# Performance work log

Hardware: AMD Instinct MI355X
Metric: run time of the kernel (lower is better)

Reference implementation:

```python
import jax, jax.numpy as jnp
import numpy as np

B, C, H, W = 2, 128, 64, 64
CR4 = C // 4  # hidden width of linear_weight / bias branches
SOFTMAX_SCALE = 1.0


def _leaky(z):
    return jnp.where(z >= 0, z, 0.2 * z)


def _conv1x1(x, w, b):
    # x: [B,Ci,H,W], w: [Co,Ci], b: [Co]
    return jnp.einsum('oc,bchw->bohw', w, x) + b[None, :, None, None]


def setup_inputs() -> dict:
    key = jax.random.key(0)
    ks = jax.random.split(key, 16)
    def n(k, shape, s=0.05):
        return jax.random.normal(k, shape, jnp.float32) * s
    return {
        'x': jax.random.normal(ks[0], (B, C, H, W), jnp.float32),
        'value_w': n(ks[1], (C, C)), 'value_b': n(ks[2], (C,)),
        'query_w': n(ks[3], (C, C)), 'query_b': n(ks[4], (C,)),
        'lw1_w': n(ks[5], (CR4, C)), 'lw1_b': n(ks[6], (CR4,)),
        'lw2_w': n(ks[7], (1, CR4)), 'lw2_b': n(ks[8], (1,)),
        'bi1_w': n(ks[9], (CR4, C)), 'bi1_b': n(ks[10], (CR4,)),
        'bi2_w': n(ks[11], (1, CR4)), 'bi2_b': n(ks[12], (1,)),
        'lin_w': n(ks[13], (C, C, 3, 3)), 'lin_b': n(ks[14], (C,)),
    }


def reference(x, value_w, value_b, query_w, query_b,
              lw1_w, lw1_b, lw2_w, lw2_b,
              bi1_w, bi1_b, bi2_w, bi2_b,
              lin_w, lin_b):
    # value / query 1x1 projections
    x1 = _conv1x1(x, value_w, value_b)   # [B,C,H,W]
    x2 = _conv1x1(x, query_w, query_b)   # [B,C,H,W]
    # dynamic per-pixel weight / bias maps (two 1x1 convs + LeakyReLU)
    wei = _conv1x1(_leaky(_conv1x1(x2, lw1_w, lw1_b)), lw2_w, lw2_b)  # [B,1,H,W]
    bii = _conv1x1(_leaky(_conv1x1(x2, bi1_w, bi1_b)), bi2_w, bi2_b)  # [B,1,H,W]

    Bn, Cn, Hn, Wn = x.shape
    L = Hn * Wn  # one 1x1 patch per spatial location (ksize=1, stride=1)
    # query patches [B,L,C]; normalize each patch to (at least 1e-4) unit norm
    wq = x2.transpose(0, 2, 3, 1).reshape(Bn, L, Cn)
    wnorm = wq / jnp.maximum(jnp.linalg.norm(wq, axis=2, keepdims=True), 1e-4)
    # attention scores: per-sample conv2d(xi, wi_normed) == batched matmul
    yi = jnp.einsum('bchw,blc->blhw', x2, wnorm)  # [B,L,H,W]
    # sparse gating
    sparse = jax.nn.relu(yi - yi.mean(axis=1, keepdims=True) * wei + bii)
    sr = (sparse != 0.0).astype(yi.dtype)
    yi = yi * sparse
    yi = jax.nn.softmax(yi * SOFTMAX_SCALE, axis=1)
    yi = jnp.maximum(yi * sr, 1e-8)
    # reconstruct with value patches (conv_transpose2d with 1x1 kernels)
    raw = x1.transpose(0, 2, 3, 1).reshape(Bn, L, Cn)
    out = jnp.einsum('blhw,blc->bchw', yi, raw)  # / (ksize*ksize) == /1
    # final 3x3 conv + LeakyReLU + residual
    y = jax.lax.conv_general_dilated(out, lin_w, (1, 1), 'SAME',
                                     dimension_numbers=('NCHW', 'OIHW', 'NCHW'))
    y = _leaky(y + lin_b[None, :, None, None])
    return y + x
```

## Files before the change

kernel.cpp:

```cpp
#include <hip/hip_runtime.h>
#include <hip/hip_bf16.h>
#include <math.h>

#define BB 2
#define C 128
#define L 4096
#define CR4 32
#define RS 4

typedef unsigned short ushort_t;
typedef __attribute__((ext_vector_type(8))) short s16x8;
typedef __attribute__((ext_vector_type(4))) float f32x4;

__device__ inline float leaky(float z) { return (z >= 0.f) ? z : 0.2f * z; }

__device__ inline unsigned short f2bf(float f) {
    unsigned int u = __builtin_bit_cast(unsigned int, f);
    unsigned int r = (u + 0x7fffu + ((u >> 16) & 1u)) >> 16;
    return (unsigned short)r;
}
__device__ inline float bf2f(unsigned short b) {
    unsigned int u = ((unsigned int)b) << 16;
    return __builtin_bit_cast(float, u);
}
__device__ inline unsigned int cvtpk(float lo, float hi) {
    unsigned int r;
    asm("v_cvt_pk_bf16_f32 %0, %1, %2" : "=v"(r) : "v"(lo), "v"(hi));
    return r;
}

__global__ __launch_bounds__(256) void k_wcomp(
    const float* __restrict__ vw, const float* __restrict__ vb,
    const float* __restrict__ qw, const float* __restrict__ qb,
    const float* __restrict__ lw1w, const float* __restrict__ lw1b,
    const float* __restrict__ bi1w, const float* __restrict__ bi1b,
    ushort_t* __restrict__ WQV, float* __restrict__ biasv)
{
    const int mt = blockIdx.x;
    const int t = threadIdx.x;
    const int kk = t >> 6, lane = t & 63;
    const int row = mt * 16 + (lane & 15);
    const int k0 = kk * 32 + (lane >> 4) * 8;
    s16x8 v;
    if (row < 128) {
        #pragma unroll
        for (int j = 0; j < 8; ++j) v[j] = (short)f2bf(vw[row * 128 + k0 + j]);
    } else if (row < 256) {
        #pragma unroll
        for (int j = 0; j < 8; ++j) v[j] = (short)f2bf(qw[(row - 128) * 128 + k0 + j]);
    } else {
        const float* w1 = (row < 288) ? lw1w + (row - 256) * 128
                                      : bi1w + (row - 288) * 128;
        float acc[8] = {0.f, 0.f, 0.f, 0.f, 0.f, 0.f, 0.f, 0.f};
        #pragma unroll 2
        for (int k = 0; k < 128; ++k) {
            float wv_ = w1[k];
            const float* qr = qw + k * 128 + k0;
            #pragma unroll
            for (int j = 0; j < 8; ++j) acc[j] = fmaf(wv_, qr[j], acc[j]);
        }
        #pragma unroll
        for (int j = 0; j < 8; ++j) v[j] = (short)f2bf(acc[j]);
    }
    *(s16x8*)(WQV + ((size_t)(mt * 4 + kk) * 64 + lane) * 8) = v;

    if (t < 16) {
        int rr = mt * 16 + t;
        float bv;
        if (rr < 128) bv = vb[rr];
        else if (rr < 256) bv = qb[rr - 128];
        else {
            const float* w1 = (rr < 288) ? lw1w + (rr - 256) * 128
                                         : bi1w + (rr - 288) * 128;
            float a = (rr < 288) ? lw1b[rr - 256] : bi1b[rr - 288];
            for (int k = 0; k < 128; ++k) a = fmaf(w1[k], qb[k], a);
            bv = a;
        }
        biasv[rr] = bv;
    }
}

__global__ __launch_bounds__(256, 1) void k_proj2(
    const float* __restrict__ x, const ushort_t* __restrict__ WQV,
    const float* __restrict__ biasv,
    const float* __restrict__ lw2w, const float* __restrict__ lw2b,
    const float* __restrict__ bi2w, const float* __restrict__ bi2b,
    ushort_t* __restrict__ x2a, ushort_t* __restrict__ x1g,
    float* __restrict__ weiA, float* __restrict__ biiA, float* __restrict__ scA,
    float* __restrict__ cpart)
{
    __shared__ __align__(16) char smem[16384 + 1536];
    char* xT = smem;
    float* biasLDS = (float*)(smem + 16384);
    float* w2LDS = biasLDS + 320;

    const int t = threadIdx.x;
    const int blk = blockIdx.x;
    const int part = blockIdx.y;
    const int b = blk >> 6;
    const int p0 = (blk & 63) * 64;
    const int wv = t >> 6, lane = t & 63, n = lane & 15, g = lane >> 4;

    biasLDS[t] = biasv[t];
    if (t < 64) {
        biasLDS[256 + t] = biasv[256 + t];
        w2LDS[t] = (t < 32) ? lw2w[t] : bi2w[t - 32];
    }

    const int pl = t & 63, cg = t >> 6;
    const float* xb = x + (size_t)b * C * L + p0 + pl;
    #pragma unroll
    for (int i = 0; i < 16; ++i) {
        int c = cg * 32 + i * 2;
        float v0 = xb[(size_t)c * L];
        float v1 = xb[(size_t)(c + 1) * L];
        int slot = c >> 3;
        int offs = (c * 2) & 15;
        int byte = pl * 256 + (((slot ^ (pl & 15)) << 4) | offs);
        *(unsigned int*)(xT + byte) = cvtpk(v0, v1);
    }
    __syncthreads();

    const int brow = wv * 16 + n;
    const int p = p0 + wv * 16 + n;
    const size_t bL = (size_t)b * L;

    if (part == 0) {
        const int mtm[12] = {0, 1, 2, 3, 4, 5, 6, 7, 16, 17, 18, 19};
        f32x4 acc[12];
        #pragma unroll
        for (int i = 0; i < 12; ++i) acc[i] = (f32x4){0.f, 0.f, 0.f, 0.f};
        #pragma unroll
        for (int kk = 0; kk < 4; ++kk) {
            const s16x8 bfr = *(const s16x8*)(xT + brow * 256 + (((4 * kk + g) ^ n) << 4));
            #pragma unroll
            for (int i = 0; i < 12; ++i) {
                const s16x8 afr = *(const s16x8*)(WQV + ((size_t)(mtm[i] * 4 + kk) * 64 + lane) * 8);
                acc[i] = __builtin_amdgcn_mfma_f32_16x16x32_bf16(afr, bfr, acc[i], 0, 0, 0);
            }
        }
        #pragma unroll
        for (int i = 0; i < 12; ++i) {
            const f32x4 bv = *(const f32x4*)(biasLDS + mtm[i] * 16 + g * 4);
            acc[i][0] += bv[0]; acc[i][1] += bv[1];
            acc[i][2] += bv[2]; acc[i][3] += bv[3];
        }
        #pragma unroll
        for (int i = 0; i < 8; ++i)
            #pragma unroll
            for (int r = 0; r < 4; ++r)
                x1g[((size_t)b * C + i * 16 + g * 4 + r) * L + p] = f2bf(acc[i][r]);
        float pw = 0.f, pbb = 0.f;
        #pragma unroll
        for (int i = 8; i < 10; ++i)
            #pragma unroll
            for (int r = 0; r < 4; ++r)
                pw = fmaf(w2LDS[(i - 8) * 16 + g * 4 + r], leaky(acc[i][r]), pw);
        #pragma unroll
        for (int i = 10; i < 12; ++i)
            #pragma unroll
            for (int r = 0; r < 4; ++r)
                pbb = fmaf(w2LDS[32 + (i - 10) * 16 + g * 4 + r], leaky(acc[i][r]), pbb);
        pw += __shfl_xor(pw, 16, 64);  pw += __shfl_xor(pw, 32, 64);
        pbb += __shfl_xor(pbb, 16, 64); pbb += __shfl_xor(pbb, 32, 64);
        if (g == 0) {
            weiA[bL + p] = pw + lw2b[0];
            biiA[bL + p] = pbb + bi2b[0];
        }
    } else {
        f32x4 acc[8];
        #pragma unroll
        for (int i = 0; i < 8; ++i) acc[i] = (f32x4){0.f, 0.f, 0.f, 0.f};
        #pragma unroll
        for (int kk = 0; kk < 4; ++kk) {
            const s16x8 bfr = *(const s16x8*)(xT + brow * 256 + (((4 * kk + g) ^ n) << 4));
            #pragma unroll
            for (int i = 0; i < 8; ++i) {
                const s16x8 afr = *(const s16x8*)(WQV + ((size_t)((8 + i) * 4 + kk) * 64 + lane) * 8);
                acc[i] = __builtin_amdgcn_mfma_f32_16x16x32_bf16(afr, bfr, acc[i], 0, 0, 0);
            }
        }
        #pragma unroll
        for (int i = 0; i < 8; ++i) {
            const f32x4 bv = *(const f32x4*)(biasLDS + (8 + i) * 16 + g * 4);
            acc[i][0] += bv[0]; acc[i][1] += bv[1];
            acc[i][2] += bv[2]; acc[i][3] += bv[3];
        }
        float pn = 0.f;
        #pragma unroll
        for (int i = 0; i < 8; ++i)
            #pragma unroll
            for (int r = 0; r < 4; ++r) pn = fmaf(acc[i][r], acc[i][r], pn);
        pn += __shfl_xor(pn, 16, 64);
        pn += __shfl_xor(pn, 32, 64);
        float scv = fmaxf(sqrtf(pn), 1e-4f);
        float dinv = 1.f / scv;
        if (g == 0) scA[bL + p] = scv;
        #pragma unroll
        for (int i = 0; i < 8; ++i) {
            uint2 uu;
            uu.x = cvtpk(acc[i][0] * dinv, acc[i][1] * dinv);
            uu.y = cvtpk(acc[i][2] * dinv, acc[i][3] * dinv);
            *(uint2*)(x2a + (bL + p) * C + i * 16 + g * 4) = uu;
        }
        float sv[32];
        #pragma unroll
        for (int i = 0; i < 8; ++i)
            #pragma unroll
            for (int r = 0; r < 4; ++r)
                sv[i * 4 + r] = acc[i][r] * dinv;
        #pragma unroll
        for (int mask = 1; mask <= 8; mask <<= 1)
            #pragma unroll
            for (int i = 0; i < 32; ++i)
                sv[i] += __shfl_xor(sv[i], mask, 64);
        __syncthreads();
        float* sumsh = (float*)xT;
        if (n == 0) {
            #pragma unroll
            for (int i = 0; i < 32; ++i) {
                int ch = (i >> 2) * 16 + g * 4 + (i & 3);
                sumsh[wv * 128 + ch] = sv[i];
            }
        }
        __syncthreads();
        if (t < 128)
            cpart[(size_t)blk * 128 + t] =
                (sumsh[t] + sumsh[128 + t]) + (sumsh[256 + t] + sumsh[384 + t]);
    }
}

__global__ __launch_bounds__(256, 2) void k_attn(
    const ushort_t* __restrict__ x2a, const ushort_t* __restrict__ x1g,
    const float* __restrict__ scA, const float* __restrict__ weiA,
    const float* __restrict__ biiA, const float* __restrict__ cpart,
    ushort_t* __restrict__ Opb, float* __restrict__ Mp, float* __restrict__ Zp)
{
    __shared__ __align__(16) char smem[73728];
    __shared__ float cbsh[128];

    const int t = threadIdx.x;
    const int w = t >> 6, lane = t & 63, n = lane & 15, g = lane >> 4;
    char* Pw = smem + 65536 + w * 2048;

    const int blk = blockIdx.x;
    const int q = blk & (RS - 1);
    const int colt = (blk >> 2) & 63;
    const int b = blk >> 8;
    const int p = colt * 64 + w * 16 + n;
    const size_t bL = (size_t)b * L;

    if (t < 128) {
        float s = 0.f;
        const float* cp = cpart + (size_t)(b * 64) * 128 + t;
        #pragma unroll 4
        for (int j = 0; j < 64; ++j) s += cp[(size_t)j * 128];
        cbsh[t] = s * (1.f / (float)L);
    }

    const int l0base = q * (L / RS);
    const char* x2src = (const char*)(x2a + (bL + l0base) * C);
    const char* x1src = (const char*)(x1g + (size_t)b * C * L);

    #define STAGE_X2(buf, tile_)                                                         \
        {   const char* sb = x2src + (size_t)(tile_) * 64 * 256;                          \
            _Pragma("unroll")                                                             \
            for (int rr = 0; rr < 4; ++rr) {                                              \
                int slot = rr * 256 + t;                                                  \
                int lrow = slot >> 4, uu = slot & 15;                                     \
                const char* gp = sb + lrow * 256 + (((uu ^ (lrow & 7))) << 4);            \
                char* lp = (buf) + ((rr * 256 + w * 64) << 4);                            \
                __builtin_amdgcn_global_load_lds(                                         \
                    (const __attribute__((address_space(1))) unsigned int*)gp,            \
                    (__attribute__((address_space(3))) unsigned int*)lp, 16, 0, 0);       \
            } }
    #define STAGE_X1(buf, l0_)                                                            \
        {   _Pragma("unroll")                                                             \
            for (int rr = 0; rr < 4; ++rr) {                                              \
                int slot = rr * 256 + t;                                                  \
                int cr = slot >> 3, uu = slot & 7;                                        \
                const char* gp = x1src + ((size_t)cr * L + (l0_) + ((uu ^ (cr & 7)) << 3)) * 2; \
                char* lp = (buf) + ((rr * 256 + w * 64) << 4);                            \
                __builtin_amdgcn_global_load_lds(                                         \
                    (const __attribute__((address_space(1))) unsigned int*)gp,            \
                    (__attribute__((address_space(3))) unsigned int*)lp, 16, 0, 0);       \
            } }

    char* Abuf0 = smem;          char* Abuf1 = smem + 16384;
    char* Xbuf0 = smem + 32768;  char* Xbuf1 = smem + 49152;

    STAGE_X2(Abuf0, 0);
    STAGE_X1(Xbuf0, l0base);
    __syncthreads();

    const s16x8* qrow = (const s16x8*)(x2a + (bL + p) * C);
    const float scp = scA[bL + p];
    s16x8 bq[4];
    float dot = 0.f;
    #pragma unroll
    for (int kk = 0; kk < 4; ++kk) {
        s16x8 raw = qrow[kk * 4 + g];
        const float* cbp = cbsh + kk * 32 + g * 8;
        s16x8 u;
        #pragma unroll
        for (int j = 0; j < 8; ++j) {
            float rv = bf2f((unsigned short)raw[j]) * scp;
            u[j] = (short)f2bf(rv);
            dot = fmaf(cbp[j], rv, dot);
        }
        bq[kk] = u;
    }
    dot += __shfl_xor(dot, 16, 64);
    dot += __shfl_xor(dot, 32, 64);
    const float tq = fmaf(weiA[bL + p], dot, -biiA[bL + p]);

    f32x4 Oacc[8];
    #pragma unroll
    for (int ct = 0; ct < 8; ++ct) Oacc[ct] = (f32x4){0.f, 0.f, 0.f, 0.f};
    float Mrun = 0.f, Zrun = 0.f;

    const int swz = n & 7;
    const int NT = L / RS / 64;

    #pragma unroll 1
    for (int tile = 0; tile < NT; ++tile) {
        char* Ab = (tile & 1) ? Abuf1 : Abuf0;
        char* Xb = (tile & 1) ? Xbuf1 : Xbuf0;
        if (tile + 1 < NT) {
            char* An = (tile & 1) ? Abuf0 : Abuf1;
            char* Xn = (tile & 1) ? Xbuf0 : Xbuf1;
            STAGE_X2(An, tile + 1);
            STAGE_X1(Xn, l0base + (tile + 1) * 64);
        }

        f32x4 s4[4];
        #pragma unroll
        for (int lt = 0; lt < 4; ++lt) s4[lt] = (f32x4){0.f, 0.f, 0.f, 0.f};
        __builtin_amdgcn_s_setprio(1);
        #pragma unroll
        for (int kk = 0; kk < 4; ++kk) {
            #pragma unroll
            for (int lt = 0; lt < 4; ++lt) {
                const s16x8 a = *(const s16x8*)(Ab + (16 * lt + n) * 256 +
                                                (((4 * kk + g) ^ swz) << 4));
                s4[lt] = __builtin_amdgcn_mfma_f32_16x16x32_bf16(a, bq[kk], s4[lt], 0, 0, 0);
            }
        }
        __builtin_amdgcn_s_setprio(0);

        float vv[16], sps[16];
        #pragma unroll
        for (int lt = 0; lt < 4; ++lt) {
            #pragma unroll
            for (int r = 0; r < 4; ++r) {
                float s = s4[lt][r];
                float sp = s - tq;
                sps[lt * 4 + r] = sp;
                vv[lt * 4 + r] = s * fmaxf(sp, 0.f);
            }
        }
        float tm[8];
        #pragma unroll
        for (int i = 0; i < 8; ++i) tm[i] = fmaxf(vv[2 * i], vv[2 * i + 1]);
        #pragma unroll
        for (int i = 0; i < 4; ++i) tm[i] = fmaxf(tm[2 * i], tm[2 * i + 1]);
        float tmax = fmaxf(fmaxf(tm[0], tm[1]), fmaxf(tm[2], tm[3]));
        tmax = fmaxf(tmax, __shfl_xor(tmax, 16, 64));
        tmax = fmaxf(tmax, __shfl_xor(tmax, 32, 64));

        if (!__all(tmax <= Mrun + 8.f)) {
            float Mn = fmaxf(Mrun, tmax);
            float so = __expf(Mrun - Mn);
            Mrun = Mn;
            Zrun *= so;
            #pragma unroll
            for (int ct = 0; ct < 8; ++ct) {
                Oacc[ct][0] *= so; Oacc[ct][1] *= so;
                Oacc[ct][2] *= so; Oacc[ct][3] *= so;
            }
        }

        #pragma unroll
        for (int lt = 0; lt < 4; ++lt) {
            float e0 = __expf(vv[lt * 4 + 0] - Mrun);
            float e1 = __expf(vv[lt * 4 + 1] - Mrun);
            float e2 = __expf(vv[lt * 4 + 2] - Mrun);
            float e3 = __expf(vv[lt * 4 + 3] - Mrun);
            Zrun += (e0 + e1) + (e2 + e3);
            float p0 = sps[lt * 4 + 0] > 0.f ? e0 : 0.f;
            float p1 = sps[lt * 4 + 1] > 0.f ? e1 : 0.f;
            float p2 = sps[lt * 4 + 2] > 0.f ? e2 : 0.f;
            float p3 = sps[lt * 4 + 3] > 0.f ? e3 : 0.f;
            int ulog = 2 * lt + (g >> 1);
            int byte = n * 128 + ((ulog ^ swz) << 4) + ((g & 1) << 3);
            uint2 uu;
            uu.x = cvtpk(p0, p1);
            uu.y = cvtpk(p2, p3);
            *(uint2*)(Pw + byte) = uu;
        }

        __builtin_amdgcn_s_setprio(1);
        #pragma unroll
        for (int kk2 = 0; kk2 < 2; ++kk2) {
            const s16x8 pb = *(const s16x8*)(Pw + n * 128 + (((4 * kk2 + g) ^ swz) << 4));
            #pragma unroll
            for (int ct = 0; ct < 8; ++ct) {
                const s16x8 a = *(const s16x8*)(Xb + (16 * ct + n) * 128 +
                                                (((4 * kk2 + g) ^ swz) << 4));
                Oacc[ct] = __builtin_amdgcn_mfma_f32_16x16x32_bf16(a, pb, Oacc[ct], 0, 0, 0);
            }
        }
        __builtin_amdgcn_s_setprio(0);
        __syncthreads();
    }
    #undef STAGE_X2
    #undef STAGE_X1

    float z = Zrun;
    z += __shfl_xor(z, 16, 64);
    z += __shfl_xor(z, 32, 64);

    const size_t sset = (size_t)(q * BB + b);
    ushort_t* ob = Opb + (sset * L + p) * C;
    #pragma unroll
    for (int ct = 0; ct < 8; ++ct) {
        uint2 uu;
        uu.x = cvtpk(Oacc[ct][0], Oacc[ct][1]);
        uu.y = cvtpk(Oacc[ct][2], Oacc[ct][3]);
        *(uint2*)(ob + 16 * ct + 4 * g) = uu;
    }
    if (g == 0) {
        Mp[sset * L + p] = Mrun;
        Zp[sset * L + p] = z;
    }
}

__global__ __launch_bounds__(256) void k_mergewrep(
    const ushort_t* __restrict__ Opb, const float* __restrict__ Mp,
    const float* __restrict__ Zp, ushort_t* __restrict__ attnb,
    const float* __restrict__ lw, ushort_t* __restrict__ W3)
{
    const int blkid = blockIdx.x;
    const int t = threadIdx.x;
    if (blkid < 1024) {
        const int idx = blkid * 256 + t;
        const int c4 = idx & 31;
        const int p = (idx >> 5) & 4095;
        const int b = idx >> 17;
        size_t is[RS];
        float M = -1e30f;
        float Mq[RS], Zq[RS];
        #pragma unroll
        for (int q = 0; q < RS; ++q) {
            is[q] = (size_t)(q * BB + b) * L + p;
            Mq[q] = Mp[is[q]];
            Zq[q] = Zp[is[q]];
            M = fmaxf(M, Mq[q]);
        }
        float Zt = 0.f;
        float aq[RS];
        #pragma unroll
        for (int q = 0; q < RS; ++q) {
            aq[q] = __expf(Mq[q] - M);
            Zt = fmaf(Zq[q], aq[q], Zt);
        }
        float zi = 1.f / Zt;
        float r0 = 0.f, r1 = 0.f, r2 = 0.f, r3 = 0.f;
        #pragma unroll
        for (int q = 0; q < RS; ++q) {
            float s = aq[q] * zi;
            const ushort4 o = *(const ushort4*)(Opb + is[q] * C + c4 * 4);
            r0 = fmaf(bf2f(o.x), s, r0);
            r1 = fmaf(bf2f(o.y), s, r1);
            r2 = fmaf(bf2f(o.z), s, r2);
            r3 = fmaf(bf2f(o.w), s, r3);
        }
        uint2 uu;
        uu.x = cvtpk(r0, r1);
        uu.y = cvtpk(r2, r3);
        *(uint2*)(attnb + ((size_t)b * L + p) * C + c4 * 4) = uu;
    } else {
        const int tid = (blkid - 1024) * 256 + t;
        const int s = tid >> 9;
        const int r = tid & 511;
        const int mt = r >> 6, lane = r & 63;
        const int co = mt * 16 + (lane & 15), g = lane >> 4;
        const int kk = s >> 2, kc = s & 3;
        const int ci0 = kc * 32 + g * 8;
        s16x8 v;
        #pragma unroll
        for (int j = 0; j < 8; ++j)
            v[j] = (short)f2bf(lw[((size_t)co * 128 + ci0 + j) * 9 + kk]);
        *(s16x8*)(W3 + (size_t)tid * 8) = v;
    }
}

__global__ __launch_bounds__(256, 1) void k_conv(
    const ushort_t* __restrict__ attnb, const float* __restrict__ x,
    const ushort_t* __restrict__ W3, const float* __restrict__ lb,
    float* __restrict__ out)
{
    __shared__ __align__(16) char attnT[49152];

    const int t = threadIdx.x;
    const int wv = t >> 6, lane = t & 63, n = lane & 15, g = lane >> 4;
    const int h = blockIdx.x;
    const int half = blockIdx.y;
    const int b = blockIdx.z;

    const char* asrc = (const char*)attnb + ((size_t)b * L + (size_t)(h - 1) * 64) * C * 2;
    #pragma unroll
    for (int rr = 0; rr < 3; ++rr) {
        if ((unsigned)(h - 1 + rr) < 64u) {
            #pragma unroll
            for (int qq = 0; qq < 4; ++qq) {
                int slot = rr * 1024 + qq * 256 + t;
                int lrow = slot >> 4, uu = slot & 15;
                const char* gp = asrc + lrow * 256 + ((uu ^ (lrow & 7)) << 4);
                char* lp = attnT + ((rr * 1024 + qq * 256 + wv * 64) << 4);
                __builtin_amdgcn_global_load_lds(
                    (const __attribute__((address_space(1))) unsigned int*)gp,
                    (__attribute__((address_space(3))) unsigned int*)lp, 16, 0, 0);
            }
        }
    }

    #define WROW(s_, mi_) (*(const s16x8*)(W3 + (((size_t)(s_) * 8 + 2 * wv + (mi_)) * 64 + lane) * 8))

    s16x8 w0a = WROW(0, 0), w0b = WROW(0, 1);
    s16x8 w1a = WROW(1, 0), w1b = WROW(1, 1);

    __syncthreads();

    f32x4 acc[2][2];
    #pragma unroll
    for (int mi = 0; mi < 2; ++mi)
        #pragma unroll
        for (int nt = 0; nt < 2; ++nt) acc[mi][nt] = (f32x4){0.f, 0.f, 0.f, 0.f};

    const s16x8 zer = {0, 0, 0, 0, 0, 0, 0, 0};

    #define CONV_STEP(s_, af0_, af1_)                                                    \
    {   const int kk = (s_) >> 2, kc = (s_) & 3;                                         \
        const int kh = kk / 3, kw = kk - kh * 3;                                         \
        const int dh = kh - 1, dw = kw - 1;                                              \
        const bool hval = ((unsigned)(h + dh) < 64u);                                    \
        _Pragma("unroll")                                                                \
        for (int nt = 0; nt < 2; ++nt) {                                                 \
            int pl = half * 32 + nt * 16 + n;                                            \
            int wd = pl + dw;                                                            \
            bool val = hval && ((unsigned)wd < 64u);                                     \
            int wc = wd < 0 ? 0 : (wd > 63 ? 63 : wd);                                   \
            int lrow = (dh + 1) * 64 + wc;                                               \
            s16x8 bf_ = *(const s16x8*)(attnT + lrow * 256 +                             \
                                        (((kc * 4 + g) ^ (lrow & 7)) << 4));             \
            if (!val) bf_ = zer;                                                         \
            acc[0][nt] = __builtin_amdgcn_mfma_f32_16x16x32_bf16(af0_, bf_, acc[0][nt], 0, 0, 0); \
            acc[1][nt] = __builtin_amdgcn_mfma_f32_16x16x32_bf16(af1_, bf_, acc[1][nt], 0, 0, 0); \
        }                                                                                \
    }

    #pragma unroll 1
    for (int s = 0; s < 36; s += 2) {
        s16x8 af0 = w0a, af1 = w0b;
        if (s + 2 < 36) { w0a = WROW(s + 2, 0); w0b = WROW(s + 2, 1); }
        CONV_STEP(s, af0, af1)
        af0 = w1a; af1 = w1b;
        if (s + 3 < 36) { w1a = WROW(s + 3, 0); w1b = WROW(s + 3, 1); }
        CONV_STEP(s + 1, af0, af1)
    }
    #undef CONV_STEP
    #undef WROW

    const float* xb = x + (size_t)b * C * L + h * 64;
    float* ob = out + (size_t)b * C * L + h * 64;
    #pragma unroll
    for (int mi = 0; mi < 2; ++mi) {
        #pragma unroll
        for (int r = 0; r < 4; ++r) {
            int co = (2 * wv + mi) * 16 + g * 4 + r;
            float bias = lb[co];
            #pragma unroll
            for (int nt = 0; nt < 2; ++nt) {
                int p_ = half * 32 + nt * 16 + n;
                float v = leaky(acc[mi][nt][r] + bias);
                ob[(size_t)co * L + p_] = v + xb[(size_t)co * L + p_];
            }
        }
    }
}

extern "C" void kernel_launch(void* const* d_in, const int* in_sizes, int n_in,
                              void* d_out, int out_size, void* d_ws, size_t ws_size,
                              hipStream_t stream) {
    const float* x     = (const float*)d_in[0];
    const float* vw    = (const float*)d_in[1];
    const float* vb    = (const float*)d_in[2];
    const float* qw    = (const float*)d_in[3];
    const float* qb    = (const float*)d_in[4];
    const float* lw1w  = (const float*)d_in[5];
    const float* lw1b  = (const float*)d_in[6];
    const float* lw2w  = (const float*)d_in[7];
    const float* lw2b  = (const float*)d_in[8];
    const float* bi1w  = (const float*)d_in[9];
    const float* bi1b  = (const float*)d_in[10];
    const float* bi2w  = (const float*)d_in[11];
    const float* bi2b  = (const float*)d_in[12];
    const float* lw    = (const float*)d_in[13];
    const float* lb    = (const float*)d_in[14];
    float* out = (float*)d_out;

    char* ws = (char*)d_ws;
    ushort_t* x2a  = (ushort_t*)ws;
    ushort_t* x1g  = (ushort_t*)(ws + 2097152);
    ushort_t* Opb  = (ushort_t*)(ws + 4194304);
    ushort_t* WQV  = (ushort_t*)(ws + 4194304);
    float* biasv = (float*)(ws + 4194304 + 81920);
    float* weiA  = (float*)(ws + 12582912);
    float* biiA  = weiA + BB * L;
    float* scA   = biiA + BB * L;
    float* Mp    = scA + BB * L;
    float* Zp    = Mp + RS * BB * L;
    float* cpart = Zp + RS * BB * L;
    ushort_t* W3 = x1g;
    ushort_t* attnb = x2a;

    hipLaunchKernelGGL(k_wcomp, dim3(20), dim3(256), 0, stream,
                       vw, vb, qw, qb, lw1w, lw1b, bi1w, bi1b, WQV, biasv);

    hipLaunchKernelGGL(k_proj2, dim3(128, 2), dim3(256), 0, stream,
                       x, WQV, biasv, lw2w, lw2b, bi2w, bi2b,
                       x2a, x1g, weiA, biiA, scA, cpart);

    hipLaunchKernelGGL(k_attn, dim3(BB * 64 * RS), dim3(256), 0, stream,
                       x2a, x1g, scA, weiA, biiA, cpart, Opb, Mp, Zp);

    hipLaunchKernelGGL(k_mergewrep, dim3(1096), dim3(256), 0, stream,
                       Opb, Mp, Zp, attnb, lw, W3);

    hipLaunchKernelGGL(k_conv, dim3(64, 2, BB), dim3(256), 0, stream,
                       attnb, x, W3, lb, out);
}
```

Before: 99.51 us.

## Give each attention wave two query column groups to reuse staged tiles

The attention kernel now runs 128 threads per block, and each wave handles two 16-query column groups (A and B) instead of one. The key and value LDS fragments are loaded into registers once per tile and reused for both query sets, which halves LDS reads per unit of MFMA work. The price is much higher register pressure (two sets of output accumulators plus 32 cached fragments) and launch bounds reduced to one block. Fewer waves per block also means each thread stages twice as many global-to-LDS loads.

```diff
diff --git a/kernel.cpp b/kernel.cpp
--- a/kernel.cpp
+++ b/kernel.cpp
@@ -230,7 +230,7 @@
     }
 }
 
-__global__ __launch_bounds__(256, 2) void k_attn(
+__global__ __launch_bounds__(128, 1) void k_attn(
     const ushort_t* __restrict__ x2a, const ushort_t* __restrict__ x1g,
     const float* __restrict__ scA, const float* __restrict__ weiA,
     const float* __restrict__ biiA, const float* __restrict__ cpart,
@@ -241,22 +241,16 @@
 
     const int t = threadIdx.x;
     const int w = t >> 6, lane = t & 63, n = lane & 15, g = lane >> 4;
-    char* Pw = smem + 65536 + w * 2048;
+    char* PwA = smem + 65536 + (w * 2) * 2048;
+    char* PwB = PwA + 2048;
 
     const int blk = blockIdx.x;
     const int q = blk & (RS - 1);
     const int colt = (blk >> 2) & 63;
     const int b = blk >> 8;
-    const int p = colt * 64 + w * 16 + n;
+    const int pA = colt * 64 + w * 16 + n;
+    const int pB = pA + 32;
     const size_t bL = (size_t)b * L;
-
-    if (t < 128) {
-        float s = 0.f;
-        const float* cp = cpart + (size_t)(b * 64) * 128 + t;
-        #pragma unroll 4
-        for (int j = 0; j < 64; ++j) s += cp[(size_t)j * 128];
-        cbsh[t] = s * (1.f / (float)L);
-    }
 
     const int l0base = q * (L / RS);
     const char* x2src = (const char*)(x2a + (bL + l0base) * C);
@@ -265,22 +259,22 @@
     #define STAGE_X2(buf, tile_)                                                         \
         {   const char* sb = x2src + (size_t)(tile_) * 64 * 256;                          \
             _Pragma("unroll")                                                             \
-            for (int rr = 0; rr < 4; ++rr) {                                              \
-                int slot = rr * 256 + t;                                                  \
+            for (int rr = 0; rr < 8; ++rr) {                                              \
+                int slot = rr * 128 + t;                                                  \
                 int lrow = slot >> 4, uu = slot & 15;                                     \
                 const char* gp = sb + lrow * 256 + (((uu ^ (lrow & 7))) << 4);            \
-                char* lp = (buf) + ((rr * 256 + w * 64) << 4);                            \
+                char* lp = (buf) + ((rr * 128 + w * 64) << 4);                            \
                 __builtin_amdgcn_global_load_lds(                                         \
                     (const __attribute__((address_space(1))) unsigned int*)gp,            \
                     (__attribute__((address_space(3))) unsigned int*)lp, 16, 0, 0);       \
             } }
     #define STAGE_X1(buf, l0_)                                                            \
         {   _Pragma("unroll")                                                             \
-            for (int rr = 0; rr < 4; ++rr) {                                              \
-                int slot = rr * 256 + t;                                                  \
+            for (int rr = 0; rr < 8; ++rr) {                                              \
+                int slot = rr * 128 + t;                                                  \
                 int cr = slot >> 3, uu = slot & 7;                                        \
                 const char* gp = x1src + ((size_t)cr * L + (l0_) + ((uu ^ (cr & 7)) << 3)) * 2; \
-                char* lp = (buf) + ((rr * 256 + w * 64) << 4);                            \
+                char* lp = (buf) + ((rr * 128 + w * 64) << 4);                            \
                 __builtin_amdgcn_global_load_lds(                                         \
                     (const __attribute__((address_space(1))) unsigned int*)gp,            \
                     (__attribute__((address_space(3))) unsigned int*)lp, 16, 0, 0);       \
@@ -291,36 +285,128 @@
 
     STAGE_X2(Abuf0, 0);
     STAGE_X1(Xbuf0, l0base);
+
+    {
+        float s = 0.f;
+        const float* cp = cpart + (size_t)(b * 64) * 128 + t;
+        #pragma unroll 4
+        for (int j = 0; j < 64; ++j) s += cp[(size_t)j * 128];
+        cbsh[t] = s * (1.f / (float)L);
+    }
     __syncthreads();
 
-    const s16x8* qrow = (const s16x8*)(x2a + (bL + p) * C);
-    const float scp = scA[bL + p];
-    s16x8 bq[4];
-    float dot = 0.f;
+    s16x8 bqA[4], bqB[4];
+    float tqA, tqB;
+    {
+        const s16x8* qrow = (const s16x8*)(x2a + (bL + pA) * C);
+        const float scp = scA[bL + pA];
+        float dot = 0.f;
+        #pragma unroll
+        for (int kk = 0; kk < 4; ++kk) {
+            s16x8 raw = qrow[kk * 4 + g];
+            const float* cbp = cbsh + kk * 32 + g * 8;
+            s16x8 u;
+            #pragma unroll
+            for (int j = 0; j < 8; ++j) {
+                float rv = bf2f((unsigned short)raw[j]) * scp;
+                u[j] = (short)f2bf(rv);
+                dot = fmaf(cbp[j], rv, dot);
+            }
+            bqA[kk] = u;
+        }
+        dot += __shfl_xor(dot, 16, 64);
+        dot += __shfl_xor(dot, 32, 64);
+        tqA = fmaf(weiA[bL + pA], dot, -biiA[bL + pA]);
+    }
+    {
+        const s16x8* qrow = (const s16x8*)(x2a + (bL + pB) * C);
+        const float scp = scA[bL + pB];
+        float dot = 0.f;
+        #pragma unroll
+        for (int kk = 0; kk < 4; ++kk) {
+            s16x8 raw = qrow[kk * 4 + g];
+            const float* cbp = cbsh + kk * 32 + g * 8;
+            s16x8 u;
+            #pragma unroll
+            for (int j = 0; j < 8; ++j) {
+                float rv = bf2f((unsigned short)raw[j]) * scp;
+                u[j] = (short)f2bf(rv);
+                dot = fmaf(cbp[j], rv, dot);
+            }
+            bqB[kk] = u;
+        }
+        dot += __shfl_xor(dot, 16, 64);
+        dot += __shfl_xor(dot, 32, 64);
+        tqB = fmaf(weiA[bL + pB], dot, -biiA[bL + pB]);
+    }
+
+    f32x4 OA[8], OB[8];
     #pragma unroll
-    for (int kk = 0; kk < 4; ++kk) {
-        s16x8 raw = qrow[kk * 4 + g];
-        const float* cbp = cbsh + kk * 32 + g * 8;
-        s16x8 u;
-        #pragma unroll
-        for (int j = 0; j < 8; ++j) {
-            float rv = bf2f((unsigned short)raw[j]) * scp;
-            u[j] = (short)f2bf(rv);
-            dot = fmaf(cbp[j], rv, dot);
-        }
-        bq[kk] = u;
-    }
-    dot += __shfl_xor(dot, 16, 64);
-    dot += __shfl_xor(dot, 32, 64);
-    const float tq = fmaf(weiA[bL + p], dot, -biiA[bL + p]);
-
-    f32x4 Oacc[8];
-    #pragma unroll
-    for (int ct = 0; ct < 8; ++ct) Oacc[ct] = (f32x4){0.f, 0.f, 0.f, 0.f};
-    float Mrun = 0.f, Zrun = 0.f;
+    for (int ct = 0; ct < 8; ++ct) {
+        OA[ct] = (f32x4){0.f, 0.f, 0.f, 0.f};
+        OB[ct] = (f32x4){0.f, 0.f, 0.f, 0.f};
+    }
+    float MrunA = 0.f, ZrunA = 0.f, MrunB = 0.f, ZrunB = 0.f;
 
     const int swz = n & 7;
     const int NT = L / RS / 64;
+
+    #define SOFTPV(sX, tqX, MrunX, ZrunX, OX, PwX)                                       \
+    {   float vv[16], sps[16];                                                           \
+        _Pragma("unroll")                                                                \
+        for (int lt = 0; lt < 4; ++lt) {                                                 \
+            _Pragma("unroll")                                                            \
+            for (int r = 0; r < 4; ++r) {                                                \
+                float s_ = sX[lt][r];                                                    \
+                float sp = s_ - tqX;                                                     \
+                sps[lt * 4 + r] = sp;                                                    \
+                vv[lt * 4 + r] = s_ * fmaxf(sp, 0.f);                                    \
+            }                                                                            \
+        }                                                                                \
+        float tm[8];                                                                     \
+        _Pragma("unroll")                                                                \
+        for (int i = 0; i < 8; ++i) tm[i] = fmaxf(vv[2 * i], vv[2 * i + 1]);             \
+        _Pragma("unroll")                                                                \
+        for (int i = 0; i < 4; ++i) tm[i] = fmaxf(tm[2 * i], tm[2 * i + 1]);             \
+        float tmax = fmaxf(fmaxf(tm[0], tm[1]), fmaxf(tm[2], tm[3]));                    \
+        tmax = fmaxf(tmax, __shfl_xor(tmax, 16, 64));                                    \
+        tmax = fmaxf(tmax, __shfl_xor(tmax, 32, 64));                                    \
+        if (!__all(tmax <= MrunX + 8.f)) {                                               \
+            float Mn = fmaxf(MrunX, tmax);                                               \
+            float so = __expf(MrunX - Mn);                                               \
+            MrunX = Mn;                                                                  \
+            ZrunX *= so;                                                                 \
+            _Pragma("unroll")                                                            \
+            for (int ct = 0; ct < 8; ++ct) {                                             \
+                OX[ct][0] *= so; OX[ct][1] *= so;                                        \
+                OX[ct][2] *= so; OX[ct][3] *= so;                                        \
+            }                                                                            \
+        }                                                                                \
+        _Pragma("unroll")                                                                \
+        for (int lt = 0; lt < 4; ++lt) {                                                 \
+            float e0 = __expf(vv[lt * 4 + 0] - MrunX);                                   \
+            float e1 = __expf(vv[lt * 4 + 1] - MrunX);                                   \
+            float e2 = __expf(vv[lt * 4 + 2] - MrunX);                                   \
+            float e3 = __expf(vv[lt * 4 + 3] - MrunX);                                   \
+            ZrunX += (e0 + e1) + (e2 + e3);                                              \
+            float p0_ = sps[lt * 4 + 0] > 0.f ? e0 : 0.f;                                \
+            float p1_ = sps[lt * 4 + 1] > 0.f ? e1 : 0.f;                                \
+            float p2_ = sps[lt * 4 + 2] > 0.f ? e2 : 0.f;                                \
+            float p3_ = sps[lt * 4 + 3] > 0.f ? e3 : 0.f;                                \
+            int ulog = 2 * lt + (g >> 1);                                                \
+            int byte = n * 128 + ((ulog ^ swz) << 4) + ((g & 1) << 3);                   \
+            *(unsigned int*)((PwX) + byte)     = cvtpk(p0_, p1_);                        \
+            *(unsigned int*)((PwX) + byte + 4) = cvtpk(p2_, p3_);                        \
+        }                                                                                \
+        _Pragma("unroll")                                                                \
+        for (int kk2 = 0; kk2 < 2; ++kk2) {                                              \
+            const s16x8 pb = *(const s16x8*)((PwX) + n * 128 + (((4 * kk2 + g) ^ swz) << 4)); \
+            _Pragma("unroll")                                                            \
+            for (int ct = 0; ct < 8; ++ct)                                               \
+                OX[ct] = __builtin_amdgcn_mfma_f32_16x16x32_bf16(xf[kk2 * 8 + ct], pb,   \
+                                                                 OX[ct], 0, 0, 0);       \
+        }                                                                                \
+    }
 
     #pragma unroll 1
     for (int tile = 0; tile < NT; ++tile) {
@@ -333,105 +419,74 @@
             STAGE_X1(Xn, l0base + (tile + 1) * 64);
         }
 
-        f32x4 s4[4];
-        #pragma unroll
-        for (int lt = 0; lt < 4; ++lt) s4[lt] = (f32x4){0.f, 0.f, 0.f, 0.f};
+        s16x8 af[16];
+        #pragma unroll
+        for (int kk = 0; kk < 4; ++kk)
+            #pragma unroll
+            for (int lt = 0; lt < 4; ++lt)
+                af[kk * 4 + lt] = *(const s16x8*)(Ab + (16 * lt + n) * 256 +
+                                                  (((4 * kk + g) ^ swz) << 4));
+        f32x4 sA[4], sB[4];
+        #pragma unroll
+        for (int lt = 0; lt < 4; ++lt) {
+            sA[lt] = (f32x4){0.f, 0.f, 0.f, 0.f};
+            sB[lt] = (f32x4){0.f, 0.f, 0.f, 0.f};
+        }
         __builtin_amdgcn_s_setprio(1);
         #pragma unroll
-        for (int kk = 0; kk < 4; ++kk) {
-            #pragma unroll
-            for (int lt = 0; lt < 4; ++lt) {
-                const s16x8 a = *(const s16x8*)(Ab + (16 * lt + n) * 256 +
-                                                (((4 * kk + g) ^ swz) << 4));
-                s4[lt] = __builtin_amdgcn_mfma_f32_16x16x32_bf16(a, bq[kk], s4[lt], 0, 0, 0);
-            }
-        }
+        for (int kk = 0; kk < 4; ++kk)
+            #pragma unroll
+            for (int lt = 0; lt < 4; ++lt)
+                sA[lt] = __builtin_amdgcn_mfma_f32_16x16x32_bf16(af[kk * 4 + lt], bqA[kk], sA[lt], 0, 0, 0);
+        #pragma unroll
+        for (int kk = 0; kk < 4; ++kk)
+            #pragma unroll
+            for (int lt = 0; lt < 4; ++lt)
+                sB[lt] = __builtin_amdgcn_mfma_f32_16x16x32_bf16(af[kk * 4 + lt], bqB[kk], sB[lt], 0, 0, 0);
         __builtin_amdgcn_s_setprio(0);
 
-        float vv[16], sps[16];
-        #pragma unroll
-        for (int lt = 0; lt < 4; ++lt) {
-            #pragma unroll
-            for (int r = 0; r < 4; ++r) {
-                float s = s4[lt][r];
-                float sp = s - tq;
-                sps[lt * 4 + r] = sp;
-                vv[lt * 4 + r] = s * fmaxf(sp, 0.f);
-            }
-        }
-        float tm[8];
-        #pragma unroll
-        for (int i = 0; i < 8; ++i) tm[i] = fmaxf(vv[2 * i], vv[2 * i + 1]);
-        #pragma unroll
-        for (int i = 0; i < 4; ++i) tm[i] = fmaxf(tm[2 * i], tm[2 * i + 1]);
-        float tmax = fmaxf(fmaxf(tm[0], tm[1]), fmaxf(tm[2], tm[3]));
-        tmax = fmaxf(tmax, __shfl_xor(tmax, 16, 64));
-        tmax = fmaxf(tmax, __shfl_xor(tmax, 32, 64));
-
-        if (!__all(tmax <= Mrun + 8.f)) {
-            float Mn = fmaxf(Mrun, tmax);
-            float so = __expf(Mrun - Mn);
-            Mrun = Mn;
-            Zrun *= so;
-            #pragma unroll
-            for (int ct = 0; ct < 8; ++ct) {
-                Oacc[ct][0] *= so; Oacc[ct][1] *= so;
-                Oacc[ct][2] *= so; Oacc[ct][3] *= so;
-            }
-        }
-
-        #pragma unroll
-        for (int lt = 0; lt < 4; ++lt) {
-            float e0 = __expf(vv[lt * 4 + 0] - Mrun);
-            float e1 = __expf(vv[lt * 4 + 1] - Mrun);
-            float e2 = __expf(vv[lt * 4 + 2] - Mrun);
-            float e3 = __expf(vv[lt * 4 + 3] - Mrun);
-            Zrun += (e0 + e1) + (e2 + e3);
-            float p0 = sps[lt * 4 + 0] > 0.f ? e0 : 0.f;
-            float p1 = sps[lt * 4 + 1] > 0.f ? e1 : 0.f;
-            float p2 = sps[lt * 4 + 2] > 0.f ? e2 : 0.f;
-            float p3 = sps[lt * 4 + 3] > 0.f ? e3 : 0.f;
-            int ulog = 2 * lt + (g >> 1);
-            int byte = n * 128 + ((ulog ^ swz) << 4) + ((g & 1) << 3);
-            uint2 uu;
-            uu.x = cvtpk(p0, p1);
-            uu.y = cvtpk(p2, p3);
-            *(uint2*)(Pw + byte) = uu;
-        }
-
-        __builtin_amdgcn_s_setprio(1);
-        #pragma unroll
-        for (int kk2 = 0; kk2 < 2; ++kk2) {
-            const s16x8 pb = *(const s16x8*)(Pw + n * 128 + (((4 * kk2 + g) ^ swz) << 4));
-            #pragma unroll
-            for (int ct = 0; ct < 8; ++ct) {
-                const s16x8 a = *(const s16x8*)(Xb + (16 * ct + n) * 128 +
-                                                (((4 * kk2 + g) ^ swz) << 4));
-                Oacc[ct] = __builtin_amdgcn_mfma_f32_16x16x32_bf16(a, pb, Oacc[ct], 0, 0, 0);
-            }
-        }
-        __builtin_amdgcn_s_setprio(0);
+        s16x8 xf[16];
+        #pragma unroll
+        for (int kk2 = 0; kk2 < 2; ++kk2)
+            #pragma unroll
+            for (int ct = 0; ct < 8; ++ct)
+                xf[kk2 * 8 + ct] = *(const s16x8*)(Xb + (16 * ct + n) * 128 +
+                                                   (((4 * kk2 + g) ^ swz) << 4));
+
+        SOFTPV(sA, tqA, MrunA, ZrunA, OA, PwA)
+        SOFTPV(sB, tqB, MrunB, ZrunB, OB, PwB)
+
         __syncthreads();
     }
+    #undef SOFTPV
     #undef STAGE_X2
     #undef STAGE_X1
 
-    float z = Zrun;
-    z += __shfl_xor(z, 16, 64);
-    z += __shfl_xor(z, 32, 64);
+    float zA = ZrunA;
+    zA += __shfl_xor(zA, 16, 64);
+    zA += __shfl_xor(zA, 32, 64);
+    float zB = ZrunB;
+    zB += __shfl_xor(zB, 16, 64);
+    zB += __shfl_xor(zB, 32, 64);
 
     const size_t sset = (size_t)(q * BB + b);
-    ushort_t* ob = Opb + (sset * L + p) * C;
+    ushort_t* obA = Opb + (sset * L + pA) * C;
+    ushort_t* obB = Opb + (sset * L + pB) * C;
     #pragma unroll
     for (int ct = 0; ct < 8; ++ct) {
-        uint2 uu;
-        uu.x = cvtpk(Oacc[ct][0], Oacc[ct][1]);
-        uu.y = cvtpk(Oacc[ct][2], Oacc[ct][3]);
-        *(uint2*)(ob + 16 * ct + 4 * g) = uu;
+        uint2 ua, ub;
+        ua.x = cvtpk(OA[ct][0], OA[ct][1]);
+        ua.y = cvtpk(OA[ct][2], OA[ct][3]);
+        ub.x = cvtpk(OB[ct][0], OB[ct][1]);
+        ub.y = cvtpk(OB[ct][2], OB[ct][3]);
+        *(uint2*)(obA + 16 * ct + 4 * g) = ua;
+        *(uint2*)(obB + 16 * ct + 4 * g) = ub;
     }
     if (g == 0) {
-        Mp[sset * L + p] = Mrun;
-        Zp[sset * L + p] = z;
+        Mp[sset * L + pA] = MrunA;
+        Zp[sset * L + pA] = zA;
+        Mp[sset * L + pB] = MrunB;
+        Zp[sset * L + pB] = zB;
     }
 }
 
@@ -632,7 +687,7 @@
                        x, WQV, biasv, lw2w, lw2b, bi2w, bi2b,
                        x2a, x1g, weiA, biiA, scA, cpart);
 
-    hipLaunchKernelGGL(k_attn, dim3(BB * 64 * RS), dim3(256), 0, stream,
+    hipLaunchKernelGGL(k_attn, dim3(BB * 64 * RS), dim3(128), 0, stream,
                        x2a, x1g, scA, weiA, biiA, cpart, Opb, Mp, Zp);
 
     hipLaunchKernelGGL(k_mergewrep, dim3(1096), dim3(256), 0, stream,
```

Measured after the change: 106.6 us. 7.1% more time.
